# Kernel tuning notes

Hardware: AMD Instinct MI355X
Metric: run time of the kernel (lower is better)

Reference implementation:

```python
import jax, jax.numpy as jnp
import numpy as np

BLOCK = 64
# NF4 codebook (normal-float 4-bit values, as in QLoRA/torchao)
NF4_TABLE = jnp.array([
    -1.0, -0.6961928009986877, -0.5250730514526367, -0.39491748809814453,
    -0.28444138169288635, -0.18477343022823334, -0.09105003625154495, 0.0,
    0.07958029955625534, 0.16093020141124725, 0.24611230194568634,
    0.33791524171829224, 0.44070982933044434, 0.5626170039176941,
    0.7229568362236023, 1.0], dtype=jnp.float32)

D_MODEL, HIDDEN = 4096, 11008
BATCH, SEQ = 2, 2048


def setup_inputs() -> dict:
    key = jax.random.key(0)
    ks = jax.random.split(key, 7)
    x = jax.random.normal(ks[0], (BATCH, SEQ, D_MODEL), dtype=jnp.float32)
    w1_q = jax.random.randint(ks[1], (HIDDEN, D_MODEL), 0, 16, dtype=jnp.int32)
    w2_q = jax.random.randint(ks[2], (HIDDEN, D_MODEL), 0, 16, dtype=jnp.int32)
    w3_q = jax.random.randint(ks[3], (D_MODEL, HIDDEN), 0, 16, dtype=jnp.int32)
    # per-block absmax scales (positive, typical weight magnitude ~0.02)
    w1_scale = jax.random.uniform(ks[4], (HIDDEN, D_MODEL // BLOCK), dtype=jnp.float32) * 0.04
    w2_scale = jax.random.uniform(ks[5], (HIDDEN, D_MODEL // BLOCK), dtype=jnp.float32) * 0.04
    w3_scale = jax.random.uniform(ks[6], (D_MODEL, HIDDEN // BLOCK), dtype=jnp.float32) * 0.04
    return {"x": x, "w1_q": w1_q, "w1_scale": w1_scale,
            "w2_q": w2_q, "w2_scale": w2_scale,
            "w3_q": w3_q, "w3_scale": w3_scale}


def dequant_nf4(q, scale):
    # q: [O, I] int codes in [0,16); scale: [O, I//BLOCK]
    O, I = q.shape
    vals = NF4_TABLE[q]                               # lookup -> [O, I]
    vals = vals.reshape(O, I // BLOCK, BLOCK) * scale[:, :, None]
    return vals.reshape(O, I)


def reference(x, w1_q, w1_scale, w2_q, w2_scale, w3_q, w3_scale):
    w1 = dequant_nf4(w1_q, w1_scale)                  # [H, D]
    w2 = dequant_nf4(w2_q, w2_scale)                  # [H, D]
    w3 = dequant_nf4(w3_q, w3_scale)                  # [D, H]
    h = jax.nn.silu(jnp.einsum('bsd,hd->bsh', x, w1)) * jnp.einsum('bsd,hd->bsh', x, w2)
    return jnp.einsum('bsh,dh->bsd', h, w3)
```

## Files before the change

### kernel.cpp

```cpp
#include <hip/hip_runtime.h>
#include <hip/hip_bf16.h>

typedef unsigned short u16;
typedef __bf16  bf16x8 __attribute__((ext_vector_type(8)));
typedef float   f32x4  __attribute__((ext_vector_type(4)));

__device__ __constant__ float NF4C[16] = {
    -1.0f, -0.6961928009986877f, -0.5250730514526367f, -0.39491748809814453f,
    -0.28444138169288635f, -0.18477343022823334f, -0.09105003625154495f, 0.0f,
    0.07958029955625534f, 0.16093020141124725f, 0.24611230194568634f,
    0.33791524171829224f, 0.44070982933044434f, 0.5626170039176941f,
    0.7229568362236023f, 1.0f };

__device__ __forceinline__ u16 f2bf(float f) {
    union { float f; unsigned u; } v; v.f = f;
    unsigned r = v.u + 0x7FFFu + ((v.u >> 16) & 1u);
    return (u16)(r >> 16);
}
__device__ __forceinline__ float bf2f(u16 b) {
    union { unsigned u; float f; } v; v.u = ((unsigned)b) << 16;
    return v.f;
}

__device__ __forceinline__ void gl2lds16(const void* g, void* l) {
    __builtin_amdgcn_global_load_lds(
        (__attribute__((address_space(1))) void*)g,
        (__attribute__((address_space(3))) void*)l,
        16, 0, 0);
}

__global__ __launch_bounds__(256) void cast_f32_bf16(
    const float* __restrict__ in, u16* __restrict__ out, int n8) {
    int i = blockIdx.x * 256 + threadIdx.x;
    if (i >= n8) return;
    const float4* p = (const float4*)in + (size_t)i * 2;
    float4 a = p[0], b = p[1];
    union { u16 u[8]; uint4 v; } r;
    r.u[0] = f2bf(a.x); r.u[1] = f2bf(a.y); r.u[2] = f2bf(a.z); r.u[3] = f2bf(a.w);
    r.u[4] = f2bf(b.x); r.u[5] = f2bf(b.y); r.u[6] = f2bf(b.z); r.u[7] = f2bf(b.w);
    ((uint4*)out)[i] = r.v;
}

__global__ __launch_bounds__(256) void dequant_nf4(
    const int* __restrict__ q, const float* __restrict__ s,
    u16* __restrict__ w, int I, int spr) {
    __shared__ float tab[16];
    if (threadIdx.x < 16) tab[threadIdx.x] = NF4C[threadIdx.x];
    __syncthreads();
    int col = (blockIdx.x * 256 + threadIdx.x) * 8;
    if (col >= I) return;
    int row = blockIdx.y;
    size_t base = (size_t)row * I + col;
    int4 c0 = *(const int4*)(q + base);
    int4 c1 = *(const int4*)(q + base + 4);
    float sc = s[(size_t)row * spr + (col >> 6)];
    union { u16 u[8]; uint4 v; } r;
    r.u[0] = f2bf(tab[c0.x & 15] * sc);
    r.u[1] = f2bf(tab[c0.y & 15] * sc);
    r.u[2] = f2bf(tab[c0.z & 15] * sc);
    r.u[3] = f2bf(tab[c0.w & 15] * sc);
    r.u[4] = f2bf(tab[c1.x & 15] * sc);
    r.u[5] = f2bf(tab[c1.y & 15] * sc);
    r.u[6] = f2bf(tab[c1.z & 15] * sc);
    r.u[7] = f2bf(tab[c1.w & 15] * sc);
    *(uint4*)(w + base) = r.v;
}

template<int EPI>
__global__ __launch_bounds__(256, 4) void gemm_bt(
    const u16* __restrict__ A, const u16* __restrict__ B,
    void* Cout, const u16* gate, int K, int ldc) {
    __shared__ u16 lA[128 * 32];
    __shared__ u16 lB[128 * 32];

    const int tid  = threadIdx.x;
    const int lane = tid & 63;
    const int wv   = tid >> 6;

    const int NT = gridDim.x, MT = gridDim.y;
    int id    = blockIdx.y * NT + blockIdx.x;
    int per   = MT << 3;
    int chunk = id / per;
    int rem   = id - chunk * per;
    int start = chunk << 3;
    int width = NT - start; if (width > 8) width = 8;
    const int bx = start + rem % width;
    const int by = rem / width;

    const int sr = lane >> 2;
    const int sq = (lane & 3) ^ ((sr >> 1) & 3);
    const int srow = wv * 16 + sr;
    const int scol = sq << 3;
    const u16* gA0 = A + (size_t)(by * 128 + srow) * K + scol;
    const u16* gA1 = gA0 + (size_t)64 * K;
    const u16* gB0 = B + (size_t)(bx * 128 + srow) * K + scol;
    const u16* gB1 = gB0 + (size_t)64 * K;
    u16* sA0 = lA + wv * 512 + lane * 8;  u16* sA1 = sA0 + 2048;
    u16* sB0 = lB + wv * 512 + lane * 8;  u16* sB1 = sB0 + 2048;

    const int r16  = lane & 15;
    const int pq   = lane >> 4;
    const int slot = (r16 << 2) + (pq ^ ((r16 >> 1) & 3));
    const int wm = (wv & 1) << 6;
    const int wn = (wv >> 1) << 6;
    const u16* fA = lA + (wv & 1) * 2048 + slot * 8;
    const u16* fB = lB + (wv >> 1) * 2048 + slot * 8;

    f32x4 acc[4][4] = {};
    const int kIters = K >> 5;
    for (int kb = 0; kb < kIters; ++kb) {
        gl2lds16(gA0, sA0);
        gl2lds16(gA1, sA1);
        gl2lds16(gB0, sB0);
        gl2lds16(gB1, sB1);
        gA0 += 32; gA1 += 32; gB0 += 32; gB1 += 32;
        __syncthreads();

        bf16x8 af[4], bfr[4];
        #pragma unroll
        for (int i = 0; i < 4; ++i) af[i]  = *(const bf16x8*)(fA + i * 512);
        #pragma unroll
        for (int j = 0; j < 4; ++j) bfr[j] = *(const bf16x8*)(fB + j * 512);
        #pragma unroll
        for (int i = 0; i < 4; ++i)
            #pragma unroll
            for (int j = 0; j < 4; ++j)
                acc[i][j] = __builtin_amdgcn_mfma_f32_16x16x32_bf16(
                    af[i], bfr[j], acc[i][j], 0, 0, 0);
        __syncthreads();
    }

    const int en = lane & 15;
    const int er = (lane >> 4) << 2;
    #pragma unroll
    for (int i = 0; i < 4; ++i) {
        int row0 = by * 128 + wm + i * 16 + er;
        #pragma unroll
        for (int j = 0; j < 4; ++j) {
            int col = bx * 128 + wn + j * 16 + en;
            #pragma unroll
            for (int r = 0; r < 4; ++r) {
                size_t idx = (size_t)(row0 + r) * ldc + col;
                float v = acc[i][j][r];
                if (EPI == 0) {
                    ((u16*)Cout)[idx] = f2bf(v);
                } else if (EPI == 1) {
                    float g = bf2f(gate[idx]);
                    float sg = g / (1.0f + __expf(-g));
                    ((u16*)Cout)[idx] = f2bf(sg * v);
                } else {
                    ((float*)Cout)[idx] = v;
                }
            }
        }
    }
}

extern "C" void kernel_launch(void* const* d_in, const int* in_sizes, int n_in,
                              void* d_out, int out_size, void* d_ws, size_t ws_size,
                              hipStream_t stream) {
    const float* x   = (const float*)d_in[0];
    const int*   w1q = (const int*)d_in[1];
    const float* w1s = (const float*)d_in[2];
    const int*   w2q = (const int*)d_in[3];
    const float* w2s = (const float*)d_in[4];
    const int*   w3q = (const int*)d_in[5];
    const float* w3s = (const float*)d_in[6];
    float* out = (float*)d_out;

    const int M = 4096, D = 4096, H = 11008;

    u16* xb = (u16*)d_ws;
    u16* wb = xb + (size_t)M * D;
    u16* hb = wb + (size_t)H * D;

    cast_f32_bf16<<<(M * D / 8 + 255) / 256, 256, 0, stream>>>(x, xb, M * D / 8);

    dim3 dqg1((D / 8 + 255) / 256, H);
    dequant_nf4<<<dqg1, 256, 0, stream>>>(w1q, w1s, wb, D, D / 64);
    gemm_bt<0><<<dim3(H / 128, M / 128), 256, 0, stream>>>(xb, wb, hb, nullptr, D, H);

    dequant_nf4<<<dqg1, 256, 0, stream>>>(w2q, w2s, wb, D, D / 64);
    gemm_bt<1><<<dim3(H / 128, M / 128), 256, 0, stream>>>(xb, wb, hb, hb, D, H);

    dim3 dqg3((H / 8 + 255) / 256, D);
    dequant_nf4<<<dqg3, 256, 0, stream>>>(w3q, w3s, wb, H, H / 64);
    gemm_bt<2><<<dim3(D / 128, M / 128), 256, 0, stream>>>(hb, wb, out, nullptr, H, D);
}
```

Baseline: 2.131 ms.

## Use 256x256 GEMM tiles with a 4-stage async LDS pipeline

The bf16 GEMM kernel moves from 128x128 tiles with 256 threads and a single LDS buffer to 256x256 tiles with 512 threads. It keeps four LDS stages filled by global_load_lds, waiting on vmcnt so loads for future k-tiles overlap the MFMA work on the current one, and raises wave priority during the MFMA burst. The block-to-tile mapping is also changed to an interleaved remap for L2 locality. The larger tiles raise arithmetic intensity and remove one barrier per k-step, at the cost of 128KB of LDS, one block per CU and higher register pressure.

```diff
diff --git a/kernel.cpp b/kernel.cpp
--- a/kernel.cpp
+++ b/kernel.cpp
@@ -28,6 +28,8 @@
         (__attribute__((address_space(3))) void*)l,
         16, 0, 0);
 }
+
+#define WAITVM(N) asm volatile("s_waitcnt vmcnt(" #N ")" ::: "memory")
 
 __global__ __launch_bounds__(256) void cast_f32_bf16(
     const float* __restrict__ in, u16* __restrict__ out, int n8) {
@@ -67,80 +69,100 @@
 }
 
 template<int EPI>
-__global__ __launch_bounds__(256, 4) void gemm_bt(
+__global__ __launch_bounds__(512, 2) void gemm_bt(
     const u16* __restrict__ A, const u16* __restrict__ B,
     void* Cout, const u16* gate, int K, int ldc) {
-    __shared__ u16 lA[128 * 32];
-    __shared__ u16 lB[128 * 32];
+    __shared__ u16 lA[4 * 8192];
+    __shared__ u16 lB[4 * 8192];
 
     const int tid  = threadIdx.x;
     const int lane = tid & 63;
     const int wv   = tid >> 6;
 
     const int NT = gridDim.x, MT = gridDim.y;
-    int id    = blockIdx.y * NT + blockIdx.x;
-    int per   = MT << 3;
-    int chunk = id / per;
-    int rem   = id - chunk * per;
-    int start = chunk << 3;
-    int width = NT - start; if (width > 8) width = 8;
-    const int bx = start + rem % width;
-    const int by = rem / width;
+    int id  = blockIdx.y * NT + blockIdx.x;
+    int nid = (id & 7) * ((NT * MT) >> 3) + (id >> 3);
+    const int bx = nid / MT;
+    const int by = nid - bx * MT;
 
     const int sr = lane >> 2;
     const int sq = (lane & 3) ^ ((sr >> 1) & 3);
-    const int srow = wv * 16 + sr;
-    const int scol = sq << 3;
-    const u16* gA0 = A + (size_t)(by * 128 + srow) * K + scol;
-    const u16* gA1 = gA0 + (size_t)64 * K;
-    const u16* gB0 = B + (size_t)(bx * 128 + srow) * K + scol;
-    const u16* gB1 = gB0 + (size_t)64 * K;
-    u16* sA0 = lA + wv * 512 + lane * 8;  u16* sA1 = sA0 + 2048;
-    u16* sB0 = lB + wv * 512 + lane * 8;  u16* sB1 = sB0 + 2048;
-
-    const int r16  = lane & 15;
-    const int pq   = lane >> 4;
-    const int slot = (r16 << 2) + (pq ^ ((r16 >> 1) & 3));
-    const int wm = (wv & 1) << 6;
-    const int wn = (wv >> 1) << 6;
-    const u16* fA = lA + (wv & 1) * 2048 + slot * 8;
-    const u16* fB = lB + (wv >> 1) * 2048 + slot * 8;
-
-    f32x4 acc[4][4] = {};
-    const int kIters = K >> 5;
-    for (int kb = 0; kb < kIters; ++kb) {
-        gl2lds16(gA0, sA0);
-        gl2lds16(gA1, sA1);
-        gl2lds16(gB0, sB0);
-        gl2lds16(gB1, sB1);
-        gA0 += 32; gA1 += 32; gB0 += 32; gB1 += 32;
-        __syncthreads();
-
-        bf16x8 af[4], bfr[4];
-        #pragma unroll
-        for (int i = 0; i < 4; ++i) af[i]  = *(const bf16x8*)(fA + i * 512);
-        #pragma unroll
-        for (int j = 0; j < 4; ++j) bfr[j] = *(const bf16x8*)(fB + j * 512);
-        #pragma unroll
-        for (int i = 0; i < 4; ++i)
-            #pragma unroll
-            for (int j = 0; j < 4; ++j)
-                acc[i][j] = __builtin_amdgcn_mfma_f32_16x16x32_bf16(
-                    af[i], bfr[j], acc[i][j], 0, 0, 0);
-        __syncthreads();
+    const u16* gA = A + (size_t)(by * 256 + wv * 16 + sr) * K + (sq << 3);
+    const u16* gB = B + (size_t)(bx * 256 + wv * 16 + sr) * K + (sq << 3);
+    const size_t half = (size_t)128 * K;
+    const int stoff = wv * 512 + lane * 8;
+
+    const int r16    = lane & 15;
+    const int pq     = lane >> 4;
+    const int slot16 = (r16 << 2) + (pq ^ ((r16 >> 1) & 3));
+    const int aFrag  = ((wv & 1) << 3) * 512 + slot16 * 8;
+    const int bFrag  = ((wv >> 1) << 2) * 512 + slot16 * 8;
+
+#define STAGE(T) do {                                                   \
+        const u16* a_ = gA + (size_t)(T) * 32;                          \
+        const u16* b_ = gB + (size_t)(T) * 32;                          \
+        u16* la_ = lA + (((T) & 3) << 13) + stoff;                      \
+        u16* lb_ = lB + (((T) & 3) << 13) + stoff;                      \
+        gl2lds16(a_, la_);                                              \
+        gl2lds16(a_ + half, la_ + 8 * 512);                             \
+        gl2lds16(b_, lb_);                                              \
+        gl2lds16(b_ + half, lb_ + 8 * 512);                             \
+    } while (0)
+
+#define COMPUTE(T) do {                                                 \
+        const u16* sa_ = lA + (((T) & 3) << 13) + aFrag;                \
+        const u16* sb_ = lB + (((T) & 3) << 13) + bFrag;                \
+        bf16x8 af[8], bfr[4];                                           \
+        _Pragma("unroll")                                               \
+        for (int i_ = 0; i_ < 8; ++i_)                                  \
+            af[i_] = *(const bf16x8*)(sa_ + i_ * 512);                  \
+        _Pragma("unroll")                                               \
+        for (int j_ = 0; j_ < 4; ++j_)                                  \
+            bfr[j_] = *(const bf16x8*)(sb_ + j_ * 512);                 \
+        __builtin_amdgcn_s_setprio(1);                                  \
+        _Pragma("unroll")                                               \
+        for (int i_ = 0; i_ < 8; ++i_)                                  \
+            _Pragma("unroll")                                           \
+            for (int j_ = 0; j_ < 4; ++j_)                              \
+                acc[i_][j_] = __builtin_amdgcn_mfma_f32_16x16x32_bf16(  \
+                    af[i_], bfr[j_], acc[i_][j_], 0, 0, 0);             \
+        __builtin_amdgcn_s_setprio(0);                                  \
+    } while (0)
+
+#define TILE_BAR() do {                                                 \
+        __builtin_amdgcn_s_barrier();                                   \
+        __builtin_amdgcn_sched_barrier(0);                              \
+    } while (0)
+
+    f32x4 acc[8][4] = {};
+    const int KT = K >> 5;
+
+    STAGE(0); STAGE(1); STAGE(2);
+
+    int t = 0;
+    for (; t < KT - 3; ++t) {
+        WAITVM(8);
+        TILE_BAR();
+        STAGE(t + 3);
+        COMPUTE(t);
     }
-
-    const int en = lane & 15;
-    const int er = (lane >> 4) << 2;
+    WAITVM(8); TILE_BAR(); COMPUTE(t); ++t;
+    WAITVM(4); TILE_BAR(); COMPUTE(t); ++t;
+    WAITVM(0); TILE_BAR(); COMPUTE(t);
+
+    const int en   = lane & 15;
+    const int er   = (lane >> 4) << 2;
+    const int row0 = by * 256 + ((wv & 1) << 7);
+    const int col0 = bx * 256 + ((wv >> 1) << 6);
     #pragma unroll
-    for (int i = 0; i < 4; ++i) {
-        int row0 = by * 128 + wm + i * 16 + er;
+    for (int i = 0; i < 8; ++i) {
+        int rowb = row0 + i * 16 + er;
         #pragma unroll
         for (int j = 0; j < 4; ++j) {
-            int col = bx * 128 + wn + j * 16 + en;
+            int col = col0 + j * 16 + en;
             #pragma unroll
             for (int r = 0; r < 4; ++r) {
-                size_t idx = (size_t)(row0 + r) * ldc + col;
+                size_t idx = (size_t)(rowb + r) * ldc + col;
                 float v = acc[i][j][r];
                 if (EPI == 0) {
                     ((u16*)Cout)[idx] = f2bf(v);
@@ -154,6 +176,9 @@
             }
         }
     }
+#undef STAGE
+#undef COMPUTE
+#undef TILE_BAR
 }
 
 extern "C" void kernel_launch(void* const* d_in, const int* in_sizes, int n_in,
@@ -178,12 +203,12 @@
 
     dim3 dqg1((D / 8 + 255) / 256, H);
     dequant_nf4<<<dqg1, 256, 0, stream>>>(w1q, w1s, wb, D, D / 64);
-    gemm_bt<0><<<dim3(H / 128, M / 128), 256, 0, stream>>>(xb, wb, hb, nullptr, D, H);
+    gemm_bt<0><<<dim3(H / 256, M / 256), 512, 0, stream>>>(xb, wb, hb, nullptr, D, H);
 
     dequant_nf4<<<dqg1, 256, 0, stream>>>(w2q, w2s, wb, D, D / 64);
-    gemm_bt<1><<<dim3(H / 128, M / 128), 256, 0, stream>>>(xb, wb, hb, hb, D, H);
+    gemm_bt<1><<<dim3(H / 256, M / 256), 512, 0, stream>>>(xb, wb, hb, hb, D, H);
 
     dim3 dqg3((H / 8 + 255) / 256, D);
     dequant_nf4<<<dqg3, 256, 0, stream>>>(w3q, w3s, wb, H, H / 64);
-    gemm_bt<2><<<dim3(D / 128, M / 128), 256, 0, stream>>>(hb, wb, out, nullptr, H, D);
-}
+    gemm_bt<2><<<dim3(D / 256, M / 256), 512, 0, stream>>>(hb, wb, out, nullptr, H, D);
+}
```

Result: faster. 2.079 ms (-2.5%).
